# Kernel tuning notes

Hardware: AMD Instinct MI355X
Metric: run time of the kernel (lower is better)

Reference implementation:

```python
import jax, jax.numpy as jnp
import numpy as np

NHEAD = 8
LAYER_NAMES = ('self', 'cross', 'self', 'cross')
EPS = 1e-6


def ln(x, g, b, eps=1e-5):
    m = jnp.mean(x, -1, keepdims=True)
    v = jnp.mean((x - m) ** 2, -1, keepdims=True)
    return (x - m) * jax.lax.rsqrt(v + eps) * g + b


def linear_attention(q, k, v, q_mask, kv_mask):
    # q: [N, L, H, D], k/v: [N, S, H, D]; LoFTR LinearAttention (elu+1 feature map)
    Q = jax.nn.elu(q) + 1.0
    K = jax.nn.elu(k) + 1.0
    if q_mask is not None:
        Q = Q * q_mask[:, :, None, None].astype(Q.dtype)
    if kv_mask is not None:
        mk = kv_mask[:, :, None, None].astype(K.dtype)
        K = K * mk
        v = v * mk
    v_len = v.shape[1]
    v = v / v_len
    KV = jnp.einsum('nshd,nshv->nhdv', K, v)
    Z = 1.0 / (jnp.einsum('nlhd,nhd->nlh', Q, K.sum(1)) + EPS)
    return jnp.einsum('nlhd,nhdv,nlh->nlhv', Q, KV, Z) * v_len


def enc_layer(x, src, q_mask, kv_mask, Wq, Wk, Wv, Wm, W1, W2, g1, b1, g2, b2):
    # x: [N, L, C], src: [N, S, C]
    N, L, C = x.shape
    S = src.shape[1]
    H, D = NHEAD, C // NHEAD
    q = (x @ Wq).reshape(N, L, H, D)
    k = (src @ Wk).reshape(N, S, H, D)
    v = (src @ Wv).reshape(N, S, H, D)
    msg = linear_attention(q, k, v, q_mask, kv_mask).reshape(N, L, C)
    msg = ln(msg @ Wm, g1, b1)
    msg = ln(jnp.tanh(jnp.concatenate([x, msg], axis=-1) @ W1) @ W2, g2, b2)
    return x + msg


def sample_descriptors(kp, fmap, s):
    # kp: [B, L, K, 2] (x, y) raw-image pixel coords; fmap: [B, C, H, W]; s: stride
    B, C, H, W = fmap.shape
    k = kp - s / 2 + 0.5
    denom = jnp.array([W * s - s / 2 - 0.5, H * s - s / 2 - 0.5], dtype=kp.dtype)
    k = (k / denom) * 2.0 - 1.0  # normalized [-1, 1]
    px = (k[..., 0] + 1.0) * 0.5 * (W - 1)  # align_corners=True grid_sample
    py = (k[..., 1] + 1.0) * 0.5 * (H - 1)
    x0 = jnp.floor(px)
    y0 = jnp.floor(py)
    wx = (px - x0)[..., None]
    wy = (py - y0)[..., None]
    x0i = jnp.clip(x0, 0, W - 1).astype(jnp.int32)
    x1i = jnp.clip(x0 + 1, 0, W - 1).astype(jnp.int32)
    y0i = jnp.clip(y0, 0, H - 1).astype(jnp.int32)
    y1i = jnp.clip(y0 + 1, 0, H - 1).astype(jnp.int32)
    fm = jnp.transpose(fmap, (0, 2, 3, 1))  # [B, H, W, C]
    bidx = jnp.arange(B)[:, None, None]
    g00 = fm[bidx, y0i, x0i]
    g01 = fm[bidx, y0i, x1i]
    g10 = fm[bidx, y1i, x0i]
    g11 = fm[bidx, y1i, x1i]
    out = (1 - wy) * ((1 - wx) * g00 + wx * g01) + wy * ((1 - wx) * g10 + wx * g11)
    # SuperPoint-style L2 normalization of sampled descriptors
    out = out / (jnp.linalg.norm(out, axis=-1, keepdims=True) + 1e-8)
    return out  # [B, L, K, C]


def geo_transformer(feat0, feat1, kp0_cross, kp1_cross, mask_self0, mask_self1,
                    mask_cross0, mask_cross1, Wq, Wk, Wv, Wm, W1, W2, g1, b1, g2, b2,
                    h0, w0, h1, w1, scale):
    B, L0, C = feat0.shape
    L1 = feat1.shape[1]
    K = kp0_cross.shape[2]
    for i, name in enumerate(LAYER_NAMES):
        p = (Wq[i], Wk[i], Wv[i], Wm[i], W1[i], W2[i], g1[i], b1[i], g2[i], b2[i])
        if name == 'self':
            # source = masked subset of x == full source with kv-mask (v_length cancels)
            feat0 = enc_layer(feat0, feat0, None, mask_self0, *p)
            feat1 = enc_layer(feat1, feat1, None, mask_self1, *p)
        else:
            fmap0 = jnp.transpose(feat0.reshape(B, h0, w0, C), (0, 3, 1, 2))
            fmap1 = jnp.transpose(feat1.reshape(B, h1, w1, C), (0, 3, 1, 2))
            f0c = sample_descriptors(kp0_cross, fmap0, scale)  # [B, L1, K, C]
            f1c = sample_descriptors(kp1_cross, fmap1, scale)  # [B, L0, K, C]
            x0 = feat0.reshape(B * L0, 1, C)
            x1 = feat1.reshape(B * L1, 1, C)
            nf0 = enc_layer(x0, f1c.reshape(B * L0, K, C), None,
                            mask_cross1.reshape(B * L0, K), *p)
            nf1 = enc_layer(x1, f0c.reshape(B * L1, K, C), None,
                            mask_cross0.reshape(B * L1, K), *p)
            feat0 = nf0.reshape(B, L0, C)
            feat1 = nf1.reshape(B, L1, C)
    return feat0, feat1


def setup_inputs() -> dict:
    key = jax.random.key(0)
    B, H0, W0, C, K, S, NL = 2, 64, 64, 256, 9, 8, 4
    L = H0 * W0
    ks = jax.random.split(key, 16)
    std = (2.0 / (C + C)) ** 0.5
    std2 = (2.0 / (2 * C + 2 * C)) ** 0.5
    std3 = (2.0 / (2 * C + C)) ** 0.5
    kp0 = jnp.stack([
        jax.random.uniform(ks[2], (B, L, K)) * (W0 * S),
        jax.random.uniform(ks[3], (B, L, K)) * (H0 * S)], axis=-1)
    kp1 = jnp.stack([
        jax.random.uniform(ks[4], (B, L, K)) * (W0 * S),
        jax.random.uniform(ks[5], (B, L, K)) * (H0 * S)], axis=-1)
    return {
        'feat0': jax.random.normal(ks[0], (B, L, C), jnp.float32),
        'feat1': jax.random.normal(ks[1], (B, L, C), jnp.float32),
        'kp0_cross': kp0.astype(jnp.float32),
        'kp1_cross': kp1.astype(jnp.float32),
        'mask_self0': jax.random.bernoulli(ks[6], 0.9, (B, L)),
        'mask_self1': jax.random.bernoulli(ks[7], 0.9, (B, L)),
        'mask_cross0': jax.random.bernoulli(ks[8], 0.8, (B, L, K)),
        'mask_cross1': jax.random.bernoulli(ks[9], 0.8, (B, L, K)),
        'Wq': jax.random.normal(ks[10], (NL, C, C), jnp.float32) * std,
        'Wk': jax.random.normal(ks[11], (NL, C, C), jnp.float32) * std,
        'Wv': jax.random.normal(ks[12], (NL, C, C), jnp.float32) * std,
        'Wm': jax.random.normal(ks[13], (NL, C, C), jnp.float32) * std,
        'W1': jax.random.normal(ks[14], (NL, 2 * C, 2 * C), jnp.float32) * std2,
        'W2': jax.random.normal(ks[15], (NL, 2 * C, C), jnp.float32) * std3,
        'g1': jnp.ones((NL, C), jnp.float32),
        'b1': jnp.zeros((NL, C), jnp.float32),
        'g2': jnp.ones((NL, C), jnp.float32),
        'b2': jnp.zeros((NL, C), jnp.float32),
        'h0': H0, 'w0': W0, 'h1': H0, 'w1': W0, 'scale': S,
    }


def reference(feat0, feat1, kp0_cross, kp1_cross, mask_self0, mask_self1,
              mask_cross0, mask_cross1, Wq, Wk, Wv, Wm, W1, W2, g1, b1, g2, b2,
              h0, w0, h1, w1, scale):
    return geo_transformer(feat0, feat1, kp0_cross, kp1_cross, mask_self0, mask_self1,
                           mask_cross0, mask_cross1, Wq, Wk, Wv, Wm, W1, W2,
                           g1, b1, g2, b2, h0, w0, h1, w1, scale)
```

## Files before the change

kernel.cpp:

```cpp
#include <hip/hip_runtime.h>
#include <cstddef>


#define NROWS 16384

typedef unsigned short ushort_t;
typedef __attribute__((ext_vector_type(8))) short short8;
typedef __attribute__((ext_vector_type(4))) float f32x4;
typedef __attribute__((ext_vector_type(4))) unsigned short ushort4_t;
typedef __attribute__((ext_vector_type(8))) unsigned short ushort8_t;
typedef _Float16 half_t;
typedef __attribute__((ext_vector_type(4))) _Float16 half4;
typedef __attribute__((ext_vector_type(8))) _Float16 half8;

__device__ __forceinline__ float b2f(unsigned short u) {
    union { unsigned int i; float f; } v; v.i = (unsigned int)u << 16; return v.f;
}
__device__ __forceinline__ unsigned short f2b(float x) {
    union { float f; unsigned int i; } v; v.f = x;
    unsigned int r = v.i + 0x7fffu + ((v.i >> 16) & 1u);
    return (unsigned short)(r >> 16);
}
__device__ __forceinline__ ushort_t f2h(float x) {
    union { half_t h; ushort_t u; } v; v.h = (half_t)x; return v.u;
}
__device__ __forceinline__ float elu1(float x) {
    return x > 0.f ? x + 1.f : __expf(x);
}

#define ASYNC_COPY16(gptr, lptr) \
    __builtin_amdgcn_global_load_lds((const __attribute__((address_space(1))) void*)(gptr), \
                                     (__attribute__((address_space(3))) void*)(lptr), 16, 0, 0)


__global__ __launch_bounds__(256) void gemm_bf16_kernel(
    const ushort_t* __restrict__ A0, int lda0,
    const ushort_t* __restrict__ Wt, int ldw,
    ushort_t* __restrict__ C, int ldc, int Kd,
    float* __restrict__ zbuf, int znf4)
{
    __shared__ ushort_t As[128 * 64];
    __shared__ ushort_t Bs[128 * 64];

    int tid = threadIdx.x;
    int m0 = blockIdx.y * 128;
    int n0 = blockIdx.x * 128;
    int lane = tid & 63, w = tid >> 6;
    int wrow = w >> 1, wcol = w & 1;
    int quad = lane >> 4, l16 = lane & 15;

    if (zbuf && blockIdx.y == 0) {
        int nblk = gridDim.x;
        for (int i = blockIdx.x * 256 + tid; i < znf4; i += nblk * 256)
            *(float4*)&zbuf[(size_t)i * 4] = (float4){0.f, 0.f, 0.f, 0.f};
    }

    f32x4 acc[4][4];
    #pragma unroll
    for (int i = 0; i < 4; i++)
        #pragma unroll
        for (int j = 0; j < 4; j++) acc[i][j] = (f32x4){0.f, 0.f, 0.f, 0.f};

    for (int kb = 0; kb < Kd; kb += 64) {
        #pragma unroll
        for (int q = 0; q < 4; q++) {
            int s = q * 256 + tid;
            int kk = s >> 9, p = s & 511;
            int row = p >> 2, c4 = p & 3;
            ASYNC_COPY16(A0 + (size_t)(m0 + row) * lda0 + kb + kk * 32 + c4 * 8,
                         (char*)As + s * 16);
        }
        #pragma unroll
        for (int q = 0; q < 4; q++) {
            int s = q * 256 + tid;
            int kk = s >> 9, p = s & 511;
            int rg = p >> 6, gi = p & 63;
            ASYNC_COPY16(Wt + (((size_t)((kb >> 5) + kk) * 48 + (n0 >> 4) + rg) * 512 + gi * 8),
                         (char*)Bs + s * 16);
        }
        __syncthreads();

        #pragma unroll
        for (int kk = 0; kk < 2; kk++) {
            short8 af[4], bf[4];
            #pragma unroll
            for (int mt = 0; mt < 4; mt++)
                af[mt] = *(const short8*)&As[kk * 4096 + (wrow * 64 + mt * 16 + l16) * 32 + quad * 8];
            #pragma unroll
            for (int nt = 0; nt < 4; nt++)
                bf[nt] = *(const short8*)&Bs[kk * 4096 + (wcol * 4 + nt) * 512 + (quad * 16 + l16) * 8];
            #pragma unroll
            for (int mt = 0; mt < 4; mt++)
                #pragma unroll
                for (int nt = 0; nt < 4; nt++)
                    acc[mt][nt] = __builtin_amdgcn_mfma_f32_16x16x32_bf16(
                        af[mt], bf[nt], acc[mt][nt], 0, 0, 0);
        }
        __syncthreads();
    }

    #pragma unroll
    for (int mt = 0; mt < 4; mt++) {
        int row = m0 + wrow * 64 + mt * 16 + quad * 4;
        #pragma unroll
        for (int nt = 0; nt < 4; nt++) {
            int col = n0 + wcol * 64 + nt * 16 + l16;
            #pragma unroll
            for (int r = 0; r < 4; r++)
                C[(size_t)(row + r) * ldc + col] = f2h(acc[mt][nt][r]);
        }
    }
}

__global__ __launch_bounds__(256) void mlp_ln_fused_kernel(
    const ushort_t* __restrict__ MSG, const ushort_t* __restrict__ Wmt,
    const float* __restrict__ g1, const float* __restrict__ b1,
    const ushort_t* __restrict__ Xb,
    const ushort_t* __restrict__ W1t, const ushort_t* __restrict__ W2t,
    const float* __restrict__ g2, const float* __restrict__ bp,
    ushort_t* __restrict__ XbfOut, const float* __restrict__ Xin,
    float* __restrict__ Xout)
{
    __shared__ ushort_t XB[32 * 256];
    __shared__ ushort_t L1s[32 * 256];
    __shared__ ushort_t Tnp[32 * 128];
    __shared__ ushort_t Bs[256 * 64];
    __shared__ ushort_t As[32 * 64];
    __shared__ float stats[256];

    int tid = threadIdx.x;
    int m0 = blockIdx.x * 32;
    int lane = tid & 63, w = tid >> 6;
    int quad = lane >> 4, l16 = lane & 15;

    #pragma unroll
    for (int i = 0; i < 4; i++) {
        int s = i * 256 + tid;
        int row = s >> 5, gp = s & 31;
        int gsrc = gp ^ (row & 7);
        ASYNC_COPY16(Xb + (size_t)(m0 + row) * 256 + gsrc * 8,
                     (char*)XB + s * 16);
    }

    f32x4 accA[2][4];
    #pragma unroll
    for (int i = 0; i < 2; i++)
        #pragma unroll
        for (int j = 0; j < 4; j++) accA[i][j] = (f32x4){0.f, 0.f, 0.f, 0.f};

    for (int kb = 0; kb < 256; kb += 64) {
        {
            int s = tid;
            int kk = s >> 7, p = s & 127;
            ASYNC_COPY16(MSG + (size_t)(m0 + (p >> 2)) * 256 + kb + kk * 32 + (p & 3) * 8,
                         (char*)As + s * 16);
        }
        #pragma unroll
        for (int q = 0; q < 8; q++) {
            int s = q * 256 + tid;
            int kk = s >> 10, p = s & 1023;
            int rg = p >> 6, gi = p & 63;
            ASYNC_COPY16(Wmt + (((size_t)((kb >> 5) + kk) * 16 + rg) * 512 + gi * 8),
                         (char*)Bs + s * 16);
        }
        __syncthreads();

        #pragma unroll
        for (int kk = 0; kk < 2; kk++) {
            short8 af[2], bf[4];
            #pragma unroll
            for (int mt = 0; mt < 2; mt++)
                af[mt] = *(const short8*)&As[kk * 1024 + (mt * 16 + l16) * 32 + quad * 8];
            #pragma unroll
            for (int nt = 0; nt < 4; nt++)
                bf[nt] = *(const short8*)&Bs[kk * 8192 + (w * 4 + nt) * 512 + (quad * 16 + l16) * 8];
            #pragma unroll
            for (int mt = 0; mt < 2; mt++)
                #pragma unroll
                for (int nt = 0; nt < 4; nt++)
                    accA[mt][nt] = __builtin_amdgcn_mfma_f32_16x16x32_bf16(
                        af[mt], bf[nt], accA[mt][nt], 0, 0, 0);
        }
        __syncthreads();
    }

    #pragma unroll
    for (int mt = 0; mt < 2; mt++)
        #pragma unroll
        for (int r = 0; r < 4; r++) {
            float s = 0.f, q = 0.f;
            #pragma unroll
            for (int nt = 0; nt < 4; nt++) {
                float v = accA[mt][nt][r];
                s += v; q += v * v;
            }
            #pragma unroll
            for (int off = 1; off < 16; off <<= 1) {
                s += __shfl_xor(s, off, 64);
                q += __shfl_xor(q, off, 64);
            }
            if (l16 == 0) {
                stats[w * 32 + mt * 16 + quad * 4 + r] = s;
                stats[128 + w * 32 + mt * 16 + quad * 4 + r] = q;
            }
        }
    __syncthreads();

    #pragma unroll
    for (int mt = 0; mt < 2; mt++) {
        #pragma unroll
        for (int r = 0; r < 4; r++) {
            int rl = mt * 16 + quad * 4 + r;
            float s = stats[rl] + stats[32 + rl] + stats[64 + rl] + stats[96 + rl];
            float q = stats[128 + rl] + stats[160 + rl] + stats[192 + rl] + stats[224 + rl];
            float m = s * (1.f / 256.f);
            float var = q * (1.f / 256.f) - m * m;
            float rs = rsqrtf(var + 1e-5f);
            #pragma unroll
            for (int nt = 0; nt < 4; nt++) {
                int col = w * 64 + nt * 16 + l16;
                float y = (accA[mt][nt][r] - m) * rs * g1[col] + b1[col];
                L1s[rl * 256 + (((col >> 3) ^ (rl & 7)) << 3) + (col & 7)] = f2b(y);
            }
        }
    }
    __syncthreads();

    f32x4 acc2[2][2][2];
    #pragma unroll
    for (int a = 0; a < 2; a++)
        #pragma unroll
        for (int i = 0; i < 2; i++)
            #pragma unroll
            for (int j = 0; j < 2; j++) acc2[a][i][j] = (f32x4){0.f, 0.f, 0.f, 0.f};

    #pragma unroll
    for (int np = 0; np < 4; np++) {
        f32x4 acc1[2][2];
        #pragma unroll
        for (int i = 0; i < 2; i++)
            #pragma unroll
            for (int j = 0; j < 2; j++) acc1[i][j] = (f32x4){0.f, 0.f, 0.f, 0.f};

        #pragma unroll
        for (int kb = 0; kb < 512; kb += 128) {
            #pragma unroll
            for (int q = 0; q < 8; q++) {
                int s = q * 256 + tid;
                int kk = s >> 9, p = s & 511;
                int rg = p >> 6, gi = p & 63;
                ASYNC_COPY16(W1t + (((size_t)((kb >> 5) + kk) * 32 + np * 8 + rg) * 512 + gi * 8),
                             (char*)Bs + s * 16);
            }
            __syncthreads();

            #pragma unroll
            for (int kk = 0; kk < 4; kk++) {
                short8 af[2], bfr[2];
                #pragma unroll
                for (int mt = 0; mt < 2; mt++) {
                    int row = mt * 16 + l16;
                    int k = kb + kk * 32 + quad * 8;
                    if (k < 256)
                        af[mt] = *(const short8*)&XB[row * 256 + (((k >> 3) ^ (row & 7)) << 3)];
                    else
                        af[mt] = *(const short8*)&L1s[row * 256 + ((((k - 256) >> 3) ^ (row & 7)) << 3)];
                }
                #pragma unroll
                for (int nt = 0; nt < 2; nt++)
                    bfr[nt] = *(const short8*)&Bs[kk * 4096 + (w * 2 + nt) * 512 + (quad * 16 + l16) * 8];
                #pragma unroll
                for (int mt = 0; mt < 2; mt++)
                    #pragma unroll
                    for (int nt = 0; nt < 2; nt++)
                        acc1[mt][nt] = __builtin_amdgcn_mfma_f32_16x16x32_bf16(
                            af[mt], bfr[nt], acc1[mt][nt], 0, 0, 0);
            }
            __syncthreads();
        }

        #pragma unroll
        for (int mt = 0; mt < 2; mt++)
            #pragma unroll
            for (int nt = 0; nt < 2; nt++)
                #pragma unroll
                for (int r = 0; r < 4; r++) {
                    int trow = mt * 16 + quad * 4 + r;
                    int c = w * 32 + nt * 16 + l16;
                    Tnp[trow * 128 + (((c >> 3) ^ (trow & 7)) << 3) + (c & 7)] =
                        f2b(tanhf(acc1[mt][nt][r]));
                }
        __syncthreads();

        #pragma unroll
        for (int kb2 = 0; kb2 < 128; kb2 += 64) {
            #pragma unroll
            for (int q = 0; q < 8; q++) {
                int s = q * 256 + tid;
                int kk = s >> 10, p = s & 1023;
                int rg = p >> 6, gi = p & 63;
                ASYNC_COPY16(W2t + (((size_t)(np * 4 + (kb2 >> 5) + kk) * 16 + rg) * 512 + gi * 8),
                             (char*)Bs + s * 16);
            }
            __syncthreads();

            #pragma unroll
            for (int kk = 0; kk < 2; kk++) {
                short8 af[2];
                #pragma unroll
                for (int mt = 0; mt < 2; mt++) {
                    int row = mt * 16 + l16;
                    int klocal = kb2 + kk * 32 + quad * 8;
                    af[mt] = *(const short8*)&Tnp[row * 128 + (((klocal >> 3) ^ (row & 7)) << 3)];
                }
                #pragma unroll
                for (int pass = 0; pass < 2; pass++)
                    #pragma unroll
                    for (int nt = 0; nt < 2; nt++) {
                        short8 bfr = *(const short8*)&Bs[kk * 8192 +
                            (pass * 8 + w * 2 + nt) * 512 + (quad * 16 + l16) * 8];
                        #pragma unroll
                        for (int mt = 0; mt < 2; mt++)
                            acc2[pass][mt][nt] = __builtin_amdgcn_mfma_f32_16x16x32_bf16(
                                af[mt], bfr, acc2[pass][mt][nt], 0, 0, 0);
                    }
            }
            __syncthreads();
        }
    }

    #pragma unroll
    for (int mt = 0; mt < 2; mt++)
        #pragma unroll
        for (int r = 0; r < 4; r++) {
            float s = 0.f, q = 0.f;
            #pragma unroll
            for (int pass = 0; pass < 2; pass++)
                #pragma unroll
                for (int nt = 0; nt < 2; nt++) {
                    float v = acc2[pass][mt][nt][r];
                    s += v; q += v * v;
                }
            #pragma unroll
            for (int off = 1; off < 16; off <<= 1) {
                s += __shfl_xor(s, off, 64);
                q += __shfl_xor(q, off, 64);
            }
            if (l16 == 0) {
                stats[w * 32 + mt * 16 + quad * 4 + r] = s;
                stats[128 + w * 32 + mt * 16 + quad * 4 + r] = q;
            }
        }
    __syncthreads();

    #pragma unroll
    for (int mt = 0; mt < 2; mt++) {
        #pragma unroll
        for (int r = 0; r < 4; r++) {
            int rl = mt * 16 + quad * 4 + r;
            float s = stats[rl] + stats[32 + rl] + stats[64 + rl] + stats[96 + rl];
            float q = stats[128 + rl] + stats[160 + rl] + stats[192 + rl] + stats[224 + rl];
            float m = s * (1.f / 256.f);
            float var = q * (1.f / 256.f) - m * m;
            float rs = rsqrtf(var + 1e-5f);
            size_t row = (size_t)(m0 + rl);
            #pragma unroll
            for (int pass = 0; pass < 2; pass++)
                #pragma unroll
                for (int nt = 0; nt < 2; nt++) {
                    int col = pass * 128 + w * 32 + nt * 16 + l16;
                    float y = (acc2[pass][mt][nt][r] - m) * rs * g2[col] + bp[col];
                    float xn = Xin[row * 256 + col] + y;
                    Xout[row * 256 + col] = xn;
                    XbfOut[row * 256 + col] = f2b(xn);
                }
        }
    }
}

__global__ __launch_bounds__(256) void wprep_kernel(
    const float* __restrict__ Wq, const float* __restrict__ Wk,
    const float* __restrict__ Wv, const float* __restrict__ Wm,
    const float* __restrict__ W1, const float* __restrict__ W2,
    ushort_t* __restrict__ Wqkvt, ushort_t* __restrict__ Wmt,
    ushort_t* __restrict__ W1t, ushort_t* __restrict__ W2t)
{
    int t = blockIdx.x;
    int layer = t / 640, r = t % 640;
    const float* src; ushort_t* dst;
    int ldsrc, tn, tk, n16, nbase;
    if (r < 192) {
        int grp = r / 64, rr = r % 64; tn = rr / 8; tk = rr % 8;
        src = (grp == 0 ? Wq : grp == 1 ? Wk : Wv) + (size_t)layer * 65536;
        ldsrc = 256;
        dst = Wqkvt + (size_t)layer * 196608;
        n16 = 48; nbase = grp * 256;
    } else if (r < 256) {
        int rr = r - 192; tn = rr / 8; tk = rr % 8;
        src = Wm + (size_t)layer * 65536; ldsrc = 256;
        dst = Wmt + (size_t)layer * 65536; n16 = 16; nbase = 0;
    } else if (r < 512) {
        int rr = r - 256; tn = rr / 16; tk = rr % 16;
        src = W1 + (size_t)layer * 262144; ldsrc = 512;
        dst = W1t + (size_t)layer * 262144; n16 = 32; nbase = 0;
    } else {
        int rr = r - 512; tn = rr / 16; tk = rr % 16;
        src = W2 + (size_t)layer * 131072; ldsrc = 256;
        dst = W2t + (size_t)layer * 131072; n16 = 16; nbase = 0;
    }
    int ln0 = tn * 32, k0 = tk * 32;
    __shared__ float tileS[32][33];
    int j = threadIdx.x & 31, i0 = threadIdx.x >> 5;
    #pragma unroll
    for (int p = 0; p < 4; p++) {
        int i = i0 + p * 8;
        tileS[i][j] = src[(size_t)(k0 + i) * ldsrc + ln0 + j];
    }
    __syncthreads();
    #pragma unroll
    for (int p = 0; p < 4; p++) {
        int i = i0 + p * 8;
        int n = nbase + ln0 + i, k = k0 + j;
        size_t off = ((size_t)(k >> 5) * n16 + (n >> 4)) * 512
                   + ((k >> 3) & 3) * 128 + (n & 15) * 8 + (k & 7);
        dst[off] = f2b(tileS[j][i]);
    }
}

__global__ __launch_bounds__(256) void init_kernel(
    const float* __restrict__ f0, const float* __restrict__ f1,
    float* __restrict__ X, ushort_t* __restrict__ Xbf)
{
    int idx = blockIdx.x * 256 + threadIdx.x;
    size_t e = (size_t)idx * 4;
    float4 v = (e < 2097152) ? *(const float4*)&f0[e] : *(const float4*)&f1[e - 2097152];
    *(float4*)&X[e] = v;
    ushort4_t u = { f2b(v.x), f2b(v.y), f2b(v.z), f2b(v.w) };
    *(ushort4_t*)&Xbf[e] = u;
}

__global__ __launch_bounds__(256) void kv_reduce_kernel(
    const ushort_t* __restrict__ QKV,
    const int* __restrict__ mask0, const int* __restrict__ mask1,
    float* __restrict__ KV, float* __restrict__ Ksum)
{
    int g = blockIdx.y;
    int t = g >> 4, b = (g >> 3) & 1, h = g & 7;
    const int* mask = t ? mask1 : mask0;
    int rowbase = t * 8192 + b * 4096;
    int s_begin = blockIdx.x * 256;

    __shared__ float sK[32][32];
    __shared__ float sV[32][32];

    int tid = threadIdx.x;
    int e  = tid & 31;
    int dq = tid >> 5;

    float acc[4] = {0.f, 0.f, 0.f, 0.f};
    float ks[4]  = {0.f, 0.f, 0.f, 0.f};

    for (int s0 = s_begin; s0 < s_begin + 256; s0 += 32) {
        #pragma unroll
        for (int q = 0; q < 2; q++) {
            int idx = tid + q * 256;
            int rl = idx >> 4;
            int part = idx & 15;
            int s = s0 + rl;
            size_t row = (size_t)(rowbase + s);
            float m = mask[b * 4096 + s] ? 1.f : 0.f;
            if (part < 8) {
                half4 u = *(const half4*)&QKV[row * 768 + 256 + h * 32 + part * 4];
                float4 f = { elu1((float)u[0]) * m, elu1((float)u[1]) * m,
                             elu1((float)u[2]) * m, elu1((float)u[3]) * m };
                *(float4*)&sK[rl][part * 4] = f;
            } else {
                half4 u = *(const half4*)&QKV[row * 768 + 512 + h * 32 + (part - 8) * 4];
                float4 f = { (float)u[0] * m, (float)u[1] * m,
                             (float)u[2] * m, (float)u[3] * m };
                *(float4*)&sV[rl][(part - 8) * 4] = f;
            }
        }
        __syncthreads();

        #pragma unroll
        for (int s = 0; s < 32; s++) {
            float4 kq = *(const float4*)&sK[s][dq * 4];
            float vv = sV[s][e];
            acc[0] += kq.x * vv;
            acc[1] += kq.y * vv;
            acc[2] += kq.z * vv;
            acc[3] += kq.w * vv;
            ks[0] += kq.x; ks[1] += kq.y; ks[2] += kq.z; ks[3] += kq.w;
        }
        __syncthreads();
    }

    #pragma unroll
    for (int j = 0; j < 4; j++)
        atomicAdd(&KV[(size_t)g * 1024 + (dq * 4 + j) * 32 + e], acc[j]);
    if (e == 0) {
        #pragma unroll
        for (int j = 0; j < 4; j++)
            atomicAdd(&Ksum[g * 32 + dq * 4 + j], ks[j]);
    }
}

__global__ __launch_bounds__(256) void attn_apply_kernel(
    const ushort_t* __restrict__ QKV, const float* __restrict__ KV,
    const float* __restrict__ Ksum, ushort_t* __restrict__ MSG)
{
    int row = blockIdx.x;
    int t = row >> 13, bb = (row >> 12) & 1;
    int gb = (t * 2 + bb) * 8;
    int c = threadIdx.x, h = c >> 5, e = c & 31;
    int g = gb + h;

    __shared__ float sQ[256];
    float qf = elu1((float)(*(const half_t*)&QKV[(size_t)row * 768 + c]));
    sQ[c] = qf;
    __syncthreads();

    float p = qf * Ksum[g * 32 + e];
    #pragma unroll
    for (int off = 16; off; off >>= 1) p += __shfl_xor(p, off, 32);
    float Z = 1.f / (p + 1e-6f);

    float acc = 0.f;
    #pragma unroll
    for (int d = 0; d < 32; d++)
        acc += sQ[h * 32 + d] * KV[(size_t)g * 1024 + d * 32 + e];

    MSG[(size_t)row * 256 + c] = f2b(acc * Z);
}

__global__ __launch_bounds__(256) void gram_kernel(
    const ushort_t* __restrict__ Xbf, float* __restrict__ Gm)
{
    int a = blockIdx.x * 4 + (threadIdx.x >> 6);
    int lane = threadIdx.x & 63;
    int img = a / 4225;
    int rr = a - img * 4225;
    int ay = rr / 65, ax = rr - ay * 65;
    int xa = ax > 0 ? ax - 1 : 0;
    int xb = ax < 64 ? ax : 63;
    if (ax == 0) xb = 0;
    int ya = ay > 0 ? ay - 1 : 0;
    int yb = ay < 64 ? ay : 63;
    if (ay == 0) yb = 0;

    size_t rbase = (size_t)img * 4096;
    size_t r0 = (rbase + ya * 64 + xa) * 256;
    size_t r1 = (rbase + ya * 64 + xb) * 256;
    size_t r2 = (rbase + yb * 64 + xa) * 256;
    size_t r3 = (rbase + yb * 64 + xb) * 256;

    int c4 = lane * 4;
    ushort4_t u0 = *(const ushort4_t*)&Xbf[r0 + c4];
    ushort4_t u1 = *(const ushort4_t*)&Xbf[r1 + c4];
    ushort4_t u2 = *(const ushort4_t*)&Xbf[r2 + c4];
    ushort4_t u3 = *(const ushort4_t*)&Xbf[r3 + c4];

    float p[10] = {0,0,0,0,0,0,0,0,0,0};
    #pragma unroll
    for (int j = 0; j < 4; j++) {
        float f0 = b2f(u0[j]), f1 = b2f(u1[j]), f2 = b2f(u2[j]), f3 = b2f(u3[j]);
        p[0] += f0 * f0; p[1] += f0 * f1; p[2] += f0 * f2; p[3] += f0 * f3;
        p[4] += f1 * f1; p[5] += f1 * f2; p[6] += f1 * f3;
        p[7] += f2 * f2; p[8] += f2 * f3; p[9] += f3 * f3;
    }
    #pragma unroll
    for (int k = 0; k < 10; k++)
        #pragma unroll
        for (int off = 32; off; off >>= 1) p[k] += __shfl_xor(p[k], off, 64);

    if (lane == 0) {
        #pragma unroll
        for (int k = 0; k < 10; k++) Gm[(size_t)a * 12 + k] = p[k];
    }
}

__global__ __launch_bounds__(256) void cross_fused_kernel(
    const ushort_t* __restrict__ QKV, const float* __restrict__ Gm,
    const float* __restrict__ kp0, const float* __restrict__ kp1,
    const int* __restrict__ maskc0, const int* __restrict__ maskc1,
    ushort_t* __restrict__ MSG)
{
    int wv = threadIdx.x >> 6;
    int lane = threadIdx.x & 63;
    int half = lane >> 5;
    int l32 = lane & 31;

    int blk = blockIdx.x;
    int qd = (blk & 7) >> 1;
    int within = ((blk >> 3) << 1) | (blk & 1);
    int row = qd * 4096 + within * 4 + wv;

    int t = row >> 13;
    int bl = row & 8191;
    int ts = 1 - t;
    const float* kp = ts ? kp1 : kp0;
    const int* mask = (t == 0) ? maskc1 : maskc0;
    int img = ts * 2 + (bl >> 12);
    int rb = img * 4096;
    const float* Gimg = Gm + (size_t)img * 50700;

    int c8 = l32 * 8;

    half8 qu = *(const half8*)&QKV[(size_t)row * 768 + c8];
    float qf[8];
    #pragma unroll
    for (int j = 0; j < 8; j++) qf[j] = elu1((float)qu[j]);

    float mU0, mU1, mU2, mU3, mSm;
    int mPack;
    {
        int msi = l32 % 5;
        int s9 = half + 2 * msi;
        int valid = (s9 < 9);
        int r = bl * 9 + (valid ? s9 : 0);
        mSm = (valid && mask[r] != 0) ? 1.f : 0.f;

        float2 xy = *(const float2*)&kp[(size_t)r * 2];
        float px = (xy.x - 3.5f) * (63.f / 507.5f);
        float py = (xy.y - 3.5f) * (63.f / 507.5f);
        float fx = floorf(px), fy = floorf(py);
        float wx = px - fx, wy = py - fy;
        int ix = (int)fx, iy = (int)fy;
        int xa = ix > 0 ? ix : 0;
        int xb = ix + 1 > 0 ? (ix + 1 < 63 ? ix + 1 : 63) : 0;
        int ya = iy > 0 ? iy : 0;
        int yb = iy + 1 > 0 ? (iy + 1 < 63 ? iy + 1 : 63) : 0;

        float w0 = (1.f - wy) * (1.f - wx);
        float w1 = (1.f - wy) * wx;
        float w2 = wy * (1.f - wx);
        float w3 = wy * wx;

        const float* G = &Gimg[(size_t)((iy + 1) * 65 + (ix + 1)) * 12];
        float4 ga = *(const float4*)&G[0];
        float4 gb4 = *(const float4*)&G[4];
        float2 gc = *(const float2*)&G[8];
        float ss = w0 * w0 * ga.x + w1 * w1 * gb4.x + w2 * w2 * gb4.w + w3 * w3 * gc.y
                 + 2.f * (w0 * w1 * ga.y + w0 * w2 * ga.z + w0 * w3 * ga.w
                        + w1 * w2 * gb4.y + w1 * w3 * gb4.z + w2 * w3 * gc.x);
        float inv = 1.f / (sqrtf(ss) + 1e-8f);
        mU0 = w0 * inv; mU1 = w1 * inv; mU2 = w2 * inv; mU3 = w3 * inv;

        int base = (rb + ya * 64 + xa) * 768;
        mPack = base | (xb - xa) | ((yb - ya) << 1);
    }

    int spack[5];
    float su0[5], su1[5], su2[5], su3[5], sm[5];
    int srcb = half * 32;
    #pragma unroll
    for (int si = 0; si < 5; si++) {
        int src = srcb + si;
        spack[si] = __shfl(mPack, src, 64);
        su0[si] = __shfl(mU0, src, 64);
        su1[si] = __shfl(mU1, src, 64);
        su2[si] = __shfl(mU2, src, 64);
        su3[si] = __shfl(mU3, src, 64);
        sm[si]  = __shfl(mSm, src, 64);
    }

    half8 kR[2][4], vR[2][4];

#define LOADKV(bufi, si_) do { \
        int pk = spack[si_]; \
        int dx = (pk & 1) ? 768 : 0; \
        int dy = (pk & 2) ? 49152 : 0; \
        size_t bK = (size_t)(pk & ~3) + 256 + c8; \
        size_t bV = bK + 256; \
        kR[bufi][0] = *(const half8*)&QKV[bK]; \
        kR[bufi][1] = *(const half8*)&QKV[bK + dx]; \
        kR[bufi][2] = *(const half8*)&QKV[bK + dy]; \
        kR[bufi][3] = *(const half8*)&QKV[bK + dx + dy]; \
        vR[bufi][0] = *(const half8*)&QKV[bV]; \
        vR[bufi][1] = *(const half8*)&QKV[bV + dx]; \
        vR[bufi][2] = *(const half8*)&QKV[bV + dy]; \
        vR[bufi][3] = *(const half8*)&QKV[bV + dx + dy]; \
    } while (0)

    float zsum = 0.f;
    float acc[8] = {0, 0, 0, 0, 0, 0, 0, 0};

    LOADKV(0, 0);
    #pragma unroll
    for (int si = 0; si < 5; si++) {
        int cur = si & 1;
        if (si + 1 < 5) {
            if (cur == 0) LOADKV(1, si + 1);
            else          LOADKV(0, si + 1);
        }
        float u0 = su0[si], u1 = su1[si], u2 = su2[si], u3 = su3[si];
        float p = 0.f;
        #pragma unroll
        for (int j = 0; j < 8; j++) {
            float kc = u0 * (float)kR[cur][0][j] + u1 * (float)kR[cur][1][j]
                     + u2 * (float)kR[cur][2][j] + u3 * (float)kR[cur][3][j];
            p += qf[j] * elu1(kc);
        }
        p += __shfl_xor(p, 1, 64);
        p += __shfl_xor(p, 2, 64);
        p *= sm[si];

        zsum += p;
        float pu0 = p * u0, pu1 = p * u1, pu2 = p * u2, pu3 = p * u3;
        #pragma unroll
        for (int j = 0; j < 8; j++)
            acc[j] += pu0 * (float)vR[cur][0][j] + pu1 * (float)vR[cur][1][j]
                    + pu2 * (float)vR[cur][2][j] + pu3 * (float)vR[cur][3][j];
    }
#undef LOADKV

    zsum += __shfl_xor(zsum, 32, 64);
    #pragma unroll
    for (int j = 0; j < 8; j++) acc[j] += __shfl_xor(acc[j], 32, 64);

    if (half == 0) {
        float Z = 1.f / (zsum + 1e-6f);
        ushort8_t o;
        #pragma unroll
        for (int j = 0; j < 8; j++) o[j] = f2b(acc[j] * Z);
        *(ushort8_t*)&MSG[(size_t)row * 256 + c8] = o;
    }
}


extern "C" void kernel_launch(void* const* d_in, const int* in_sizes, int n_in,
                              void* d_out, int out_size, void* d_ws, size_t ws_size,
                              hipStream_t stream)
{
    const float* feat0 = (const float*)d_in[0];
    const float* feat1 = (const float*)d_in[1];
    const float* kp0 = (const float*)d_in[2];
    const float* kp1 = (const float*)d_in[3];
    const int* ms0 = (const int*)d_in[4];
    const int* ms1 = (const int*)d_in[5];
    const int* mc0 = (const int*)d_in[6];
    const int* mc1 = (const int*)d_in[7];
    const float* Wq = (const float*)d_in[8];
    const float* Wk = (const float*)d_in[9];
    const float* Wv = (const float*)d_in[10];
    const float* Wm = (const float*)d_in[11];
    const float* W1 = (const float*)d_in[12];
    const float* W2 = (const float*)d_in[13];
    const float* g1 = (const float*)d_in[14];
    const float* b1 = (const float*)d_in[15];
    const float* g2 = (const float*)d_in[16];
    const float* b2 = (const float*)d_in[17];

    char* p = (char*)d_ws;
    float*    X     = (float*)p;            p += 16777216;
    ushort_t* Xbf   = (ushort_t*)p;         p += 8388608;
    ushort_t* QKV   = (ushort_t*)p;         p += 25165824;
    ushort_t* MSG   = (ushort_t*)p;         p += 8388608;
    ushort_t* L1bf  = (ushort_t*)p;         p += 8388608;
    float*    KVb   = (float*)p;            p += 131072;
    float*    KSb   = (float*)p;            p += 4096;
    float*    Gm    = (float*)p;            p += 811264;
    ushort_t* Wqkvt = (ushort_t*)p;         p += 1572864;
    ushort_t* Wmt   = (ushort_t*)p;         p += 524288;
    ushort_t* W1t   = (ushort_t*)p;         p += 2097152;
    ushort_t* W2t   = (ushort_t*)p;         p += 1048576;
    (void)L1bf;

    init_kernel<<<4096, 256, 0, stream>>>(feat0, feat1, X, Xbf);
    wprep_kernel<<<2560, 256, 0, stream>>>(Wq, Wk, Wv, Wm, W1, W2, Wqkvt, Wmt, W1t, W2t);

    for (int i = 0; i < 4; i++) {
        const ushort_t* Wqkvt_l = Wqkvt + (size_t)i * 196608;
        const ushort_t* Wmt_l   = Wmt   + (size_t)i * 65536;
        const ushort_t* W1t_l   = W1t   + (size_t)i * 262144;
        const ushort_t* W2t_l   = W2t   + (size_t)i * 131072;
        const float* g1_l = g1 + (size_t)i * 256;
        const float* b1_l = b1 + (size_t)i * 256;
        const float* g2_l = g2 + (size_t)i * 256;
        const float* b2_l = b2 + (size_t)i * 256;
        bool is_self = (i == 0 || i == 2);

        gemm_bf16_kernel<<<dim3(6, 128), 256, 0, stream>>>(
            Xbf, 256, Wqkvt_l, 256, QKV, 768, 256,
            is_self ? KVb : nullptr, 33792 / 4);

        if (is_self) {
            kv_reduce_kernel<<<dim3(16, 32), 256, 0, stream>>>(QKV, ms0, ms1, KVb, KSb);
            attn_apply_kernel<<<NROWS, 256, 0, stream>>>(QKV, KVb, KSb, MSG);
        } else {
            gram_kernel<<<4225, 256, 0, stream>>>(Xbf, Gm);
            cross_fused_kernel<<<NROWS / 4, 256, 0, stream>>>(QKV, Gm, kp0, kp1, mc0, mc1, MSG);
        }

        float* Xout = (i == 3) ? (float*)d_out : X;
        mlp_ln_fused_kernel<<<NROWS / 32, 256, 0, stream>>>(
            MSG, Wmt_l, g1_l, b1_l, Xbf, W1t_l, W2t_l, g2_l, b2_l, Xbf, X, Xout);
    }
}
```

Measured before the change: 564.2 us.

## Fuse next layer's QKV projection into the MLP/LayerNorm kernel epilogue

The MLP+LN kernel now keeps its bf16 output rows in shared memory and immediately computes the next layer's QKV projection for those 32 rows, writing QKV directly. This removes the separate QKV GEMM launch for layers 1-3 and the re-read of Xbf from global memory. The zeroing of the KV accumulation buffer also moves into this kernel. In exchange each block does much more work with only 512 blocks, which may lower parallelism. Weight tiles are reloaded per 32-row block, raising L2 traffic.

```diff
diff --git a/kernel.cpp b/kernel.cpp
--- a/kernel.cpp
+++ b/kernel.cpp
@@ -119,7 +119,9 @@
     const ushort_t* __restrict__ W1t, const ushort_t* __restrict__ W2t,
     const float* __restrict__ g2, const float* __restrict__ bp,
     ushort_t* __restrict__ XbfOut, const float* __restrict__ Xin,
-    float* __restrict__ Xout)
+    float* __restrict__ Xout,
+    const ushort_t* __restrict__ Wqkv, ushort_t* __restrict__ QKVout,
+    float* __restrict__ zbuf, int znf4)
 {
     __shared__ ushort_t XB[32 * 256];
     __shared__ ushort_t L1s[32 * 256];
@@ -132,6 +134,11 @@
     int m0 = blockIdx.x * 32;
     int lane = tid & 63, w = tid >> 6;
     int quad = lane >> 4, l16 = lane & 15;
+
+    if (zbuf) {
+        for (int ii = blockIdx.x * 256 + tid; ii < znf4; ii += gridDim.x * 256)
+            *(float4*)&zbuf[(size_t)ii * 4] = (float4){0.f, 0.f, 0.f, 0.f};
+    }
 
     #pragma unroll
     for (int i = 0; i < 4; i++) {
@@ -372,7 +379,66 @@
                     float y = (acc2[pass][mt][nt][r] - m) * rs * g2[col] + bp[col];
                     float xn = Xin[row * 256 + col] + y;
                     Xout[row * 256 + col] = xn;
-                    XbfOut[row * 256 + col] = f2b(xn);
+                    ushort_t xb16 = f2b(xn);
+                    XbfOut[row * 256 + col] = xb16;
+                    XB[rl * 256 + (((col >> 3) ^ (rl & 7)) << 3) + (col & 7)] = xb16;
+                }
+        }
+    }
+
+    if (Wqkv) {
+        __syncthreads();
+        #pragma unroll
+        for (int nc = 0; nc < 3; nc++) {
+            f32x4 accq[2][4];
+            #pragma unroll
+            for (int i = 0; i < 2; i++)
+                #pragma unroll
+                for (int j = 0; j < 4; j++) accq[i][j] = (f32x4){0.f, 0.f, 0.f, 0.f};
+
+            for (int kb = 0; kb < 256; kb += 64) {
+                #pragma unroll
+                for (int q = 0; q < 8; q++) {
+                    int s = q * 256 + tid;
+                    int kk = s >> 10, p = s & 1023;
+                    int rg = p >> 6, gi = p & 63;
+                    ASYNC_COPY16(Wqkv + (((size_t)((kb >> 5) + kk) * 48 + nc * 16 + rg) * 512 + gi * 8),
+                                 (char*)Bs + s * 16);
+                }
+                __syncthreads();
+
+                #pragma unroll
+                for (int kk = 0; kk < 2; kk++) {
+                    short8 af[2], bf[4];
+                    #pragma unroll
+                    for (int mt = 0; mt < 2; mt++) {
+                        int row = mt * 16 + l16;
+                        int k = kb + kk * 32 + quad * 8;
+                        af[mt] = *(const short8*)&XB[row * 256 + (((k >> 3) ^ (row & 7)) << 3)];
+                    }
+                    #pragma unroll
+                    for (int nt = 0; nt < 4; nt++)
+                        bf[nt] = *(const short8*)&Bs[kk * 8192 + (w * 4 + nt) * 512 + (quad * 16 + l16) * 8];
+                    #pragma unroll
+                    for (int mt = 0; mt < 2; mt++)
+                        #pragma unroll
+                        for (int nt = 0; nt < 4; nt++)
+                            accq[mt][nt] = __builtin_amdgcn_mfma_f32_16x16x32_bf16(
+                                af[mt], bf[nt], accq[mt][nt], 0, 0, 0);
+                }
+                __syncthreads();
+            }
+
+            #pragma unroll
+            for (int mt = 0; mt < 2; mt++)
+                #pragma unroll
+                for (int r = 0; r < 4; r++) {
+                    int rl = mt * 16 + quad * 4 + r;
+                    #pragma unroll
+                    for (int nt = 0; nt < 4; nt++) {
+                        int col = nc * 256 + w * 64 + nt * 16 + l16;
+                        QKVout[(size_t)(m0 + rl) * 768 + col] = f2h(accq[mt][nt][r]);
+                    }
                 }
         }
     }
@@ -770,8 +836,10 @@
     init_kernel<<<4096, 256, 0, stream>>>(feat0, feat1, X, Xbf);
     wprep_kernel<<<2560, 256, 0, stream>>>(Wq, Wk, Wv, Wm, W1, W2, Wqkvt, Wmt, W1t, W2t);
 
+    gemm_bf16_kernel<<<dim3(6, 128), 256, 0, stream>>>(
+        Xbf, 256, Wqkvt, 256, QKV, 768, 256, KVb, 33792 / 4);
+
     for (int i = 0; i < 4; i++) {
-        const ushort_t* Wqkvt_l = Wqkvt + (size_t)i * 196608;
         const ushort_t* Wmt_l   = Wmt   + (size_t)i * 65536;
         const ushort_t* W1t_l   = W1t   + (size_t)i * 262144;
         const ushort_t* W2t_l   = W2t   + (size_t)i * 131072;
@@ -781,10 +849,6 @@
         const float* b2_l = b2 + (size_t)i * 256;
         bool is_self = (i == 0 || i == 2);
 
-        gemm_bf16_kernel<<<dim3(6, 128), 256, 0, stream>>>(
-            Xbf, 256, Wqkvt_l, 256, QKV, 768, 256,
-            is_self ? KVb : nullptr, 33792 / 4);
-
         if (is_self) {
             kv_reduce_kernel<<<dim3(16, 32), 256, 0, stream>>>(QKV, ms0, ms1, KVb, KSb);
             attn_apply_kernel<<<NROWS, 256, 0, stream>>>(QKV, KVb, KSb, MSG);
@@ -794,7 +858,10 @@
         }
 
         float* Xout = (i == 3) ? (float*)d_out : X;
+        const ushort_t* Wqkv_next = (i < 3) ? (Wqkvt + (size_t)(i + 1) * 196608) : nullptr;
+        float* zb = (i == 1) ? KVb : nullptr;
         mlp_ln_fused_kernel<<<NROWS / 32, 256, 0, stream>>>(
-            MSG, Wmt_l, g1_l, b1_l, Xbf, W1t_l, W2t_l, g2_l, b2_l, Xbf, X, Xout);
-    }
-}
+            MSG, Wmt_l, g1_l, b1_l, Xbf, W1t_l, W2t_l, g2_l, b2_l, Xbf, X, Xout,
+            Wqkv_next, QKV, zb, 33792 / 4);
+    }
+}
```

Result: faster. 551.2 us (median of 2 runs) (-2.3%).
